# Performance work log

Hardware: AMD Instinct MI355X
Metric: run time of the kernel (lower is better)

## Reference

```python
import jax, jax.numpy as jnp
import numpy as np

N_NODES = 50000
N_EDGES = 1600000
EMB_DIM = 128
N_PATH = 2
N_LAYERS = 2
N_HEADS = 8
HEAD_DIM = EMB_DIM // N_HEADS


def setup_inputs() -> dict:
    key = jax.random.key(0)
    ks = jax.random.split(key, 6)
    fs = jax.random.normal(ks[0], (N_PATH, N_NODES, EMB_DIM), dtype=jnp.float32)
    W = jax.random.normal(ks[1], (N_PATH, N_LAYERS, EMB_DIM, EMB_DIM), dtype=jnp.float32) * (1.0 / np.sqrt(EMB_DIM))
    attn_l = jax.random.normal(ks[2], (N_PATH, N_LAYERS, N_HEADS, HEAD_DIM), dtype=jnp.float32) * 0.1
    attn_r = jax.random.normal(ks[3], (N_PATH, N_LAYERS, N_HEADS, HEAD_DIM), dtype=jnp.float32) * 0.1
    bias = jnp.zeros((N_PATH, N_LAYERS, EMB_DIM), dtype=jnp.float32)
    edges = jax.random.randint(ks[4], (N_PATH, 2, N_EDGES), 0, N_NODES, dtype=jnp.int32)
    return {"fs": fs, "W": W, "attn_l": attn_l, "attn_r": attn_r, "bias": bias, "edges": edges}


def gat_conv(h, src, dst, W, al, ar, b):
    # h: [N, F_in]; DGL GATConv, eval mode (dropout off), residual Identity, bias, ELU.
    N = h.shape[0]
    H, D = al.shape
    feat = (h @ W).reshape(N, H, D)                      # fc projection
    el = jnp.einsum('nhd,hd->nh', feat, al)              # [N, H]
    er = jnp.einsum('nhd,hd->nh', feat, ar)              # [N, H]
    e = jax.nn.leaky_relu(el[src] + er[dst], 0.2)        # [E, H]
    # edge softmax over incoming edges of each destination node
    emax = jax.ops.segment_max(e, dst, num_segments=N)   # [N, H], -inf for 0-in-degree
    emax = jnp.where(jnp.isfinite(emax), emax, 0.0)
    ex = jnp.exp(e - emax[dst])                          # [E, H]
    esum = jax.ops.segment_sum(ex, dst, num_segments=N)  # [N, H]
    alpha = ex / jnp.maximum(esum[dst], 1e-9)            # [E, H]
    msg = alpha[:, :, None] * feat[src]                  # [E, H, D]
    rst = jax.ops.segment_sum(msg, dst, num_segments=N)  # [N, H, D]
    rst = rst + h.reshape(N, H, D) + b.reshape(1, H, D)  # residual (Identity) + bias
    out = jax.nn.elu(rst)
    return out.reshape(N, H * D), alpha


def reference(fs, W, attn_l, attn_r, bias, edges):
    semantic_embeddings = []
    element_weights = []
    for p in range(N_PATH):
        h = fs[p]
        src, dst = edges[p, 0], edges[p, 1]
        attn = None
        for l in range(N_LAYERS):
            h, attn = gat_conv(h, src, dst, W[p, l], attn_l[p, l], attn_r[p, l], bias[p, l])
        semantic_embeddings.append(h)
        element_weights.append(attn)
    return jnp.stack(semantic_embeddings), jnp.stack(element_weights)
```

## Files before the change

kernel.cpp:

```cpp
#include <hip/hip_runtime.h>
#include <hip/hip_bf16.h>

#define NND 50000
#define NE  1600000
#define EMB 128
#define NH  8
#define HD  16
#define NB  98

typedef __attribute__((ext_vector_type(8))) short short8v;
typedef __attribute__((ext_vector_type(4))) float f32x4;

__device__ __forceinline__ float lrelu(float x) { return x > 0.f ? x : 0.2f * x; }
__device__ __forceinline__ float elu(float x)   { return x > 0.f ? x : expm1f(x); }

__device__ __forceinline__ unsigned short f2bf(float x) {
    __hip_bfloat16 b = __float2bfloat16(x);
    return *reinterpret_cast<unsigned short*>(&b);
}
__device__ __forceinline__ float bf2f(unsigned short u) {
    __hip_bfloat16 b = *reinterpret_cast<__hip_bfloat16*>(&u);
    return __bfloat162float(b);
}

__global__ __launch_bounds__(256) void wpack4(
    const float* __restrict__ W, unsigned short* __restrict__ bphi, unsigned short* __restrict__ bplo)
{
    int s = blockIdx.x * 256 + threadIdx.x;
    int q    = s >> 11;
    int sidx = s & 2047;
    int n    = sidx >> 8;
    int kt   = (sidx >> 6) & 3;
    int lane = sidx & 63;
    int col  = n * 16 + (lane & 15);
    int krow = kt * 32 + ((lane >> 4) << 3);
    const float* Wm = W + (size_t)q * EMB * EMB;
    #pragma unroll
    for (int j = 0; j < 8; ++j) {
        float x = Wm[(size_t)(krow + j) * EMB + col];
        unsigned short hi = f2bf(x);
        unsigned short lo = f2bf(x - bf2f(hi));
        bphi[(size_t)s * 8 + j] = hi;
        bplo[(size_t)s * 8 + j] = lo;
    }
}

__device__ __forceinline__ void gemm_epilogue(
    f32x4 acc[2][2], int lane, int wave, int rowbase,
    const float* __restrict__ alv, const float* __restrict__ arv,
    unsigned short* __restrict__ feat_bf, float* __restrict__ el, float* __restrict__ er)
{
    const int colr = lane & 15;
    const int rgrp = lane >> 4;
    #pragma unroll
    for (int m = 0; m < 2; ++m) {
        const int row0 = rowbase + m * 16 + rgrp * 4;
        #pragma unroll
        for (int q = 0; q < 2; ++q) {
            const int nn = wave * 2 + q;
            f32x4 a = acc[m][q];
            #pragma unroll
            for (int r = 0; r < 4; ++r) {
                if (row0 + r < NND)
                    feat_bf[(size_t)(row0 + r) * EMB + nn * 16 + colr] = f2bf(a[r]);
            }
            const float alc = alv[nn * 16 + colr];
            const float arc = arv[nn * 16 + colr];
            float pl[4], pr[4];
            #pragma unroll
            for (int r = 0; r < 4; ++r) { pl[r] = a[r] * alc; pr[r] = a[r] * arc; }
            #pragma unroll
            for (int mask = 1; mask < 16; mask <<= 1) {
                #pragma unroll
                for (int r = 0; r < 4; ++r) {
                    pl[r] += __shfl_xor(pl[r], mask);
                    pr[r] += __shfl_xor(pr[r], mask);
                }
            }
            if (colr == 0) {
                #pragma unroll
                for (int r = 0; r < 4; ++r) {
                    int row = row0 + r;
                    if (row < NND) {
                        el[row * NH + nn] = pl[r];
                        er[row * NH + nn] = pr[r];
                    }
                }
            }
        }
    }
}

__global__ __launch_bounds__(256) void mfma_gemm_f32(
    const float* __restrict__ fs,
    const unsigned short* __restrict__ bphi_all, const unsigned short* __restrict__ bplo_all,
    const float* __restrict__ al_all, const float* __restrict__ ar_all,
    unsigned short* __restrict__ feat_all, float* __restrict__ el_all, float* __restrict__ er_all)
{
    const int p = blockIdx.y;
    const int q4 = p * 2;
    const float* hin = fs + (size_t)p * NND * EMB;
    const unsigned short* bphi = bphi_all + (size_t)q4 * 16384;
    const unsigned short* bplo = bplo_all + (size_t)q4 * 16384;
    const float* alv = al_all + (size_t)q4 * NH * HD;
    const float* arv = ar_all + (size_t)q4 * NH * HD;
    unsigned short* feat_bf = feat_all + (size_t)p * NND * EMB;
    float* el = el_all + (size_t)p * NND * NH;
    float* er = er_all + (size_t)p * NND * NH;

    const int lane = threadIdx.x & 63;
    const int wave = threadIdx.x >> 6;
    const int rowbase = blockIdx.x * 32;

    f32x4 acc[2][2];
    #pragma unroll
    for (int m = 0; m < 2; ++m)
        #pragma unroll
        for (int q = 0; q < 2; ++q)
            acc[m][q] = (f32x4){0.f, 0.f, 0.f, 0.f};

    const int ar0 = rowbase + (lane & 15);
    const int ar1 = ar0 + 16;
    const int car0 = ar0 < NND ? ar0 : NND - 1;
    const int car1 = ar1 < NND ? ar1 : NND - 1;
    const int kofs = (lane >> 4) * 8;

    #pragma unroll
    for (int kt = 0; kt < 4; ++kt) {
        const int k0 = kt * 32 + kofs;
        short8v ah0, av0, ah1, av1;
        {
            const float4* fr = reinterpret_cast<const float4*>(hin + (size_t)car0 * EMB + k0);
            float4 x0 = fr[0], x1 = fr[1];
            float xs[8] = { x0.x, x0.y, x0.z, x0.w, x1.x, x1.y, x1.z, x1.w };
            #pragma unroll
            for (int j = 0; j < 8; ++j) {
                unsigned short hi = f2bf(xs[j]);
                ah0[j] = (short)hi;
                av0[j] = (short)f2bf(xs[j] - bf2f(hi));
            }
        }
        {
            const float4* fr = reinterpret_cast<const float4*>(hin + (size_t)car1 * EMB + k0);
            float4 x0 = fr[0], x1 = fr[1];
            float xs[8] = { x0.x, x0.y, x0.z, x0.w, x1.x, x1.y, x1.z, x1.w };
            #pragma unroll
            for (int j = 0; j < 8; ++j) {
                unsigned short hi = f2bf(xs[j]);
                ah1[j] = (short)hi;
                av1[j] = (short)f2bf(xs[j] - bf2f(hi));
            }
        }
        #pragma unroll
        for (int q = 0; q < 2; ++q) {
            const int nn = wave * 2 + q;
            const size_t bofs = ((size_t)(nn * 4 + kt) * 64 + lane) * 8;
            short8v bh = *reinterpret_cast<const short8v*>(bphi + bofs);
            short8v bl = *reinterpret_cast<const short8v*>(bplo + bofs);
            acc[0][q] = __builtin_amdgcn_mfma_f32_16x16x32_bf16(ah0, bh, acc[0][q], 0, 0, 0);
            acc[1][q] = __builtin_amdgcn_mfma_f32_16x16x32_bf16(ah1, bh, acc[1][q], 0, 0, 0);
            acc[0][q] = __builtin_amdgcn_mfma_f32_16x16x32_bf16(av0, bh, acc[0][q], 0, 0, 0);
            acc[1][q] = __builtin_amdgcn_mfma_f32_16x16x32_bf16(av1, bh, acc[1][q], 0, 0, 0);
            acc[0][q] = __builtin_amdgcn_mfma_f32_16x16x32_bf16(ah0, bl, acc[0][q], 0, 0, 0);
            acc[1][q] = __builtin_amdgcn_mfma_f32_16x16x32_bf16(ah1, bl, acc[1][q], 0, 0, 0);
        }
    }
    gemm_epilogue(acc, lane, wave, rowbase, alv, arv, feat_bf, el, er);
}

__global__ __launch_bounds__(256) void mfma_gemm_bf(
    const unsigned short* __restrict__ hhi_all, const unsigned short* __restrict__ hlo_all,
    const unsigned short* __restrict__ bphi_all, const unsigned short* __restrict__ bplo_all,
    const float* __restrict__ al_all, const float* __restrict__ ar_all,
    unsigned short* __restrict__ feat_all, float* __restrict__ el_all, float* __restrict__ er_all)
{
    const int p = blockIdx.y;
    const int q4 = p * 2 + 1;
    const unsigned short* hhi = hhi_all + (size_t)p * NND * EMB;
    const unsigned short* hlo = hlo_all + (size_t)p * NND * EMB;
    const unsigned short* bphi = bphi_all + (size_t)q4 * 16384;
    const unsigned short* bplo = bplo_all + (size_t)q4 * 16384;
    const float* alv = al_all + (size_t)q4 * NH * HD;
    const float* arv = ar_all + (size_t)q4 * NH * HD;
    unsigned short* feat_bf = feat_all + (size_t)p * NND * EMB;
    float* el = el_all + (size_t)p * NND * NH;
    float* er = er_all + (size_t)p * NND * NH;

    const int lane = threadIdx.x & 63;
    const int wave = threadIdx.x >> 6;
    const int rowbase = blockIdx.x * 32;

    f32x4 acc[2][2];
    #pragma unroll
    for (int m = 0; m < 2; ++m)
        #pragma unroll
        for (int q = 0; q < 2; ++q)
            acc[m][q] = (f32x4){0.f, 0.f, 0.f, 0.f};

    const int ar0 = rowbase + (lane & 15);
    const int ar1 = ar0 + 16;
    const int car0 = ar0 < NND ? ar0 : NND - 1;
    const int car1 = ar1 < NND ? ar1 : NND - 1;
    const int kofs = (lane >> 4) * 8;

    #pragma unroll
    for (int kt = 0; kt < 4; ++kt) {
        const int k0 = kt * 32 + kofs;
        short8v ah0 = *reinterpret_cast<const short8v*>(hhi + (size_t)car0 * EMB + k0);
        short8v av0 = *reinterpret_cast<const short8v*>(hlo + (size_t)car0 * EMB + k0);
        short8v ah1 = *reinterpret_cast<const short8v*>(hhi + (size_t)car1 * EMB + k0);
        short8v av1 = *reinterpret_cast<const short8v*>(hlo + (size_t)car1 * EMB + k0);
        #pragma unroll
        for (int q = 0; q < 2; ++q) {
            const int nn = wave * 2 + q;
            const size_t bofs = ((size_t)(nn * 4 + kt) * 64 + lane) * 8;
            short8v bh = *reinterpret_cast<const short8v*>(bphi + bofs);
            short8v bl = *reinterpret_cast<const short8v*>(bplo + bofs);
            acc[0][q] = __builtin_amdgcn_mfma_f32_16x16x32_bf16(ah0, bh, acc[0][q], 0, 0, 0);
            acc[1][q] = __builtin_amdgcn_mfma_f32_16x16x32_bf16(ah1, bh, acc[1][q], 0, 0, 0);
            acc[0][q] = __builtin_amdgcn_mfma_f32_16x16x32_bf16(av0, bh, acc[0][q], 0, 0, 0);
            acc[1][q] = __builtin_amdgcn_mfma_f32_16x16x32_bf16(av1, bh, acc[1][q], 0, 0, 0);
            acc[0][q] = __builtin_amdgcn_mfma_f32_16x16x32_bf16(ah0, bl, acc[0][q], 0, 0, 0);
            acc[1][q] = __builtin_amdgcn_mfma_f32_16x16x32_bf16(ah1, bl, acc[1][q], 0, 0, 0);
        }
    }
    gemm_epilogue(acc, lane, wave, rowbase, alv, arv, feat_bf, el, er);
}

__global__ __launch_bounds__(256) void bucket_count(
    const int* __restrict__ edges, int* __restrict__ bcnt)
{
    const int p = blockIdx.y;
    const int* dst = edges + (size_t)p * 2 * NE + NE;
    __shared__ int hist[NB];
    const int t = threadIdx.x;
    for (int b = t; b < NB; b += 256) hist[b] = 0;
    __syncthreads();
    const int e0 = blockIdx.x * 2048 + t * 8;
    #pragma unroll
    for (int j = 0; j < 8; ++j) {
        int e = e0 + j;
        if (e < NE) atomicAdd(&hist[dst[e] >> 9], 1);
    }
    __syncthreads();
    for (int b = t; b < NB; b += 256)
        if (hist[b]) atomicAdd(&bcnt[p * 128 + b], hist[b]);
}

__global__ __launch_bounds__(128) void scan_bucket(
    const int* __restrict__ bcnt, int* __restrict__ bbase, int* __restrict__ bcur)
{
    const int p = blockIdx.x;
    __shared__ int s[128];
    const int t = threadIdx.x;
    s[t] = (t < NB) ? bcnt[p * 128 + t] : 0;
    __syncthreads();
    for (int off = 1; off < 128; off <<= 1) {
        int v = (t >= off) ? s[t - off] : 0;
        __syncthreads();
        s[t] += v;
        __syncthreads();
    }
    int excl = (t > 0) ? s[t - 1] : 0;
    if (t <= NB) bbase[p * 128 + t] = excl;
    if (t < NB)  bcur[p * 128 + t]  = excl;
}

__global__ __launch_bounds__(256) void bucket_scatter(
    const int* __restrict__ edges, int* __restrict__ bcur, int* __restrict__ ebuf)
{
    const int p = blockIdx.y;
    const int* src = edges + (size_t)p * 2 * NE;
    const int* dst = src + NE;
    int* eb = ebuf + (size_t)p * NE;
    __shared__ int hist[NB];
    __shared__ int base[NB];
    __shared__ int lcur[NB];
    const int t  = threadIdx.x;
    const int e0 = blockIdx.x * 2048 + t * 8;

    for (int b = t; b < NB; b += 256) { hist[b] = 0; lcur[b] = 0; }
    __syncthreads();

    int sj[8], dj[8];
    bool vj[8];
    #pragma unroll
    for (int j = 0; j < 8; ++j) {
        int e = e0 + j;
        vj[j] = (e < NE);
        if (vj[j]) {
            sj[j] = src[e];
            dj[j] = dst[e];
            atomicAdd(&hist[dj[j] >> 9], 1);
        }
    }
    __syncthreads();
    for (int b = t; b < NB; b += 256) {
        int c = hist[b];
        base[b] = c > 0 ? atomicAdd(&bcur[p * 128 + b], c) : 0;
    }
    __syncthreads();
    #pragma unroll
    for (int j = 0; j < 8; ++j) {
        if (vj[j]) {
            int b   = dj[j] >> 9;
            int off = atomicAdd(&lcur[b], 1);
            eb[(size_t)base[b] + off] = (sj[j] << 9) | (dj[j] & 511);
        }
    }
}

__global__ __launch_bounds__(1024) void bucket_fill(
    const int* __restrict__ bbase, const int* __restrict__ ebuf,
    int* __restrict__ rowptr, int* __restrict__ csrsrc)
{
    const int p = blockIdx.y;
    const int* eb = ebuf + (size_t)p * NE;
    int* rp = rowptr + (size_t)p * (NND + 1);
    int* cs = csrsrc + (size_t)p * NE;
    __shared__ int hist[512];
    __shared__ int excl[512];
    const int b    = blockIdx.x;
    const int n0   = b << 9;
    const int t    = threadIdx.x;
    const int base = bbase[p * 128 + b];
    const int cnt  = bbase[p * 128 + b + 1] - base;

    if (t < 512) hist[t] = 0;
    __syncthreads();
    for (int i = t; i < cnt; i += 1024)
        atomicAdd(&hist[eb[base + i] & 511], 1);
    __syncthreads();
    if (t < 512) excl[t] = hist[t];
    __syncthreads();
    for (int off = 1; off < 512; off <<= 1) {
        int v = 0;
        if (t < 512 && t >= off) v = excl[t - off];
        __syncthreads();
        if (t < 512) excl[t] += v;
        __syncthreads();
    }
    if (t < 512) {
        int e = excl[t] - hist[t];
        int n = n0 + t;
        if (n < NND) rp[n] = base + e;
        hist[t] = e;
    }
    if (b == NB - 1 && t == 0) rp[NND] = NE;
    __syncthreads();
    for (int i = t; i < cnt; i += 1024) {
        int ed = eb[base + i];
        int q = atomicAdd(&hist[ed & 511], 1);
        cs[base + q] = ed >> 9;
    }
}

__global__ __launch_bounds__(256) void gather_agg(
    const int* __restrict__ rowptr_all, const int* __restrict__ csrsrc_all,
    const float* __restrict__ el_all, const float* __restrict__ er_all,
    const unsigned int* __restrict__ feat_all,
    const float* __restrict__ fs,
    const unsigned int* __restrict__ hhi_all,
    const unsigned int* __restrict__ hlo_all,
    const float* __restrict__ bias_all,
    float* __restrict__ esum_all,
    float* __restrict__ out_emb,
    int layer)
{
    const int p    = blockIdx.y;
    const int wid  = (blockIdx.x * blockDim.x + threadIdx.x) >> 6;
    const int lane = threadIdx.x & 63;
    if (wid >= NND) return;
    const int n = wid;
    const int h = lane >> 3;

    const int* rowptr = rowptr_all + (size_t)p * (NND + 1);
    const int* csrsrc = csrsrc_all + (size_t)p * NE;
    const float* el   = el_all + (size_t)p * NND * NH;
    const float* er   = er_all + (size_t)p * NND * NH;
    const unsigned int* featu = feat_all + (size_t)p * NND * 64;
    const float* bias = bias_all + (size_t)(p * 2 + layer) * EMB;

    const float ern = er[n * NH + h];
    const int r0 = __builtin_amdgcn_readfirstlane(rowptr[n]);
    const int r1 = __builtin_amdgcn_readfirstlane(rowptr[n + 1]);

    float acc0 = 0.f, acc1 = 0.f, es = 0.f;

    int i = r0;
    for (; i + 16 <= r1; i += 16) {
        int sj[16];
        #pragma unroll
        for (int j = 0; j < 16; ++j) sj[j] = csrsrc[i + j];
        unsigned int vs[16];
        #pragma unroll
        for (int j = 0; j < 16; ++j) vs[j] = featu[(size_t)sj[j] * 64 + lane];
        float w[16];
        #pragma unroll
        for (int j = 0; j < 16; ++j) w[j] = __expf(lrelu(el[sj[j] * NH + h] + ern));
        #pragma unroll
        for (int j = 0; j < 16; ++j) {
            es  += w[j];
            acc0 = fmaf(w[j], __uint_as_float(vs[j] << 16), acc0);
            acc1 = fmaf(w[j], __uint_as_float(vs[j] & 0xffff0000u), acc1);
        }
    }
    if (i + 8 <= r1) {
        int sj[8];
        #pragma unroll
        for (int j = 0; j < 8; ++j) sj[j] = csrsrc[i + j];
        unsigned int vs[8];
        #pragma unroll
        for (int j = 0; j < 8; ++j) vs[j] = featu[(size_t)sj[j] * 64 + lane];
        #pragma unroll
        for (int j = 0; j < 8; ++j) {
            float w = __expf(lrelu(el[sj[j] * NH + h] + ern));
            es  += w;
            acc0 = fmaf(w, __uint_as_float(vs[j] << 16), acc0);
            acc1 = fmaf(w, __uint_as_float(vs[j] & 0xffff0000u), acc1);
        }
        i += 8;
    }
    for (; i < r1; ++i) {
        int sj = csrsrc[i];
        unsigned int v = featu[(size_t)sj * 64 + lane];
        float w = __expf(lrelu(el[sj * NH + h] + ern));
        es  += w;
        acc0 = fmaf(w, __uint_as_float(v << 16), acc0);
        acc1 = fmaf(w, __uint_as_float(v & 0xffff0000u), acc1);
    }

    if ((lane & 7) == 0) esum_all[((size_t)p * NND + n) * NH + h] = es;
    const float inv = 1.f / fmaxf(es, 1e-9f);

    float h0, h1;
    if (layer == 0) {
        float2 hv = reinterpret_cast<const float2*>(fs + (size_t)p * NND * EMB)[(size_t)n * 64 + lane];
        h0 = hv.x; h1 = hv.y;
    } else {
        unsigned int hiu = hhi_all[((size_t)p * NND + n) * 64 + lane];
        unsigned int lou = hlo_all[((size_t)p * NND + n) * 64 + lane];
        h0 = __uint_as_float(hiu << 16) + __uint_as_float(lou << 16);
        h1 = __uint_as_float(hiu & 0xffff0000u) + __uint_as_float(lou & 0xffff0000u);
    }
    float o0 = elu(fmaf(acc0, inv, h0 + bias[lane * 2]));
    float o1 = elu(fmaf(acc1, inv, h1 + bias[lane * 2 + 1]));

    if (layer == 1) {
        reinterpret_cast<float2*>(out_emb + (size_t)p * NND * EMB)[(size_t)n * 64 + lane] =
            make_float2(o0, o1);
    } else {
        unsigned short hi0 = f2bf(o0), hi1 = f2bf(o1);
        unsigned short lo0 = f2bf(o0 - bf2f(hi0)), lo1 = f2bf(o1 - bf2f(hi1));
        const size_t idx = ((size_t)p * NND + n) * 64 + lane;
        const_cast<unsigned int*>(hhi_all)[idx] = (unsigned int)hi0 | ((unsigned int)hi1 << 16);
        const_cast<unsigned int*>(hlo_all)[idx] = (unsigned int)lo0 | ((unsigned int)lo1 << 16);
    }
}

__global__ __launch_bounds__(256) void alpha_write8(
    const int* __restrict__ edges,
    const float* __restrict__ el_all, const float* __restrict__ er_all,
    const float* __restrict__ esum_all, float* __restrict__ out_alpha)
{
    const int p = blockIdx.y;
    int e = blockIdx.x * 256 + threadIdx.x;
    if (e >= NE) return;
    const int* src = edges + (size_t)p * 2 * NE;
    const int* dst = src + NE;
    const float* el   = el_all   + (size_t)p * NND * NH;
    const float* er   = er_all   + (size_t)p * NND * NH;
    const float* esum = esum_all + (size_t)p * NND * NH;
    int s = src[e], d = dst[e];
    const float4* el4 = reinterpret_cast<const float4*>(el + (size_t)s * 8);
    const float4* er4 = reinterpret_cast<const float4*>(er + (size_t)d * 8);
    const float4* es4 = reinterpret_cast<const float4*>(esum + (size_t)d * 8);
    float4 L0 = el4[0], L1 = el4[1];
    float4 R0 = er4[0], R1 = er4[1];
    float4 S0 = es4[0], S1 = es4[1];
    float4 a0, a1;
    a0.x = __fdividef(__expf(lrelu(L0.x + R0.x)), fmaxf(S0.x, 1e-9f));
    a0.y = __fdividef(__expf(lrelu(L0.y + R0.y)), fmaxf(S0.y, 1e-9f));
    a0.z = __fdividef(__expf(lrelu(L0.z + R0.z)), fmaxf(S0.z, 1e-9f));
    a0.w = __fdividef(__expf(lrelu(L0.w + R0.w)), fmaxf(S0.w, 1e-9f));
    a1.x = __fdividef(__expf(lrelu(L1.x + R1.x)), fmaxf(S1.x, 1e-9f));
    a1.y = __fdividef(__expf(lrelu(L1.y + R1.y)), fmaxf(S1.y, 1e-9f));
    a1.z = __fdividef(__expf(lrelu(L1.z + R1.z)), fmaxf(S1.z, 1e-9f));
    a1.w = __fdividef(__expf(lrelu(L1.w + R1.w)), fmaxf(S1.w, 1e-9f));
    float4* o4 = reinterpret_cast<float4*>(out_alpha + ((size_t)p * NE + e) * 8);
    o4[0] = a0;
    o4[1] = a1;
}

extern "C" void kernel_launch(void* const* d_in, const int* in_sizes, int n_in,
                              void* d_out, int out_size, void* d_ws, size_t ws_size,
                              hipStream_t stream) {
    const float* fs   = (const float*)d_in[0];
    const float* W    = (const float*)d_in[1];
    const float* al   = (const float*)d_in[2];
    const float* ar   = (const float*)d_in[3];
    const float* bias = (const float*)d_in[4];
    const int*   edges= (const int*)d_in[5];

    float* out       = (float*)d_out;
    float* out_emb   = out;
    float* out_alpha = out + (size_t)2 * NND * EMB;

    char* ws = (char*)d_ws;
    auto take = [&](size_t bytes) {
        char* r = ws;
        ws += (bytes + 15) & ~(size_t)15;
        return r;
    };
    unsigned short* feat_bf = (unsigned short*)take((size_t)2 * NND * EMB * 2);
    unsigned short* hhi     = (unsigned short*)take((size_t)2 * NND * EMB * 2);
    unsigned short* hlo     = (unsigned short*)take((size_t)2 * NND * EMB * 2);
    float*          el      = (float*)take((size_t)2 * NND * NH * 4);
    float*          er      = (float*)take((size_t)2 * NND * NH * 4);
    float*          esum    = (float*)take((size_t)2 * NND * NH * 4);
    int*            rowptr  = (int*)take((size_t)2 * (NND + 1) * 4);
    int*            bcnt    = (int*)take((size_t)2 * 128 * 4);
    int*            bbase   = (int*)take((size_t)2 * 128 * 4);
    int*            bcur    = (int*)take((size_t)2 * 128 * 4);
    int*            csrsrc  = (int*)take((size_t)2 * NE * 4);
    unsigned short* bphi    = (unsigned short*)take((size_t)4 * 16384 * 2);
    unsigned short* bplo    = (unsigned short*)take((size_t)4 * 16384 * 2);

    int*          ebuf  = (int*)hlo;
    unsigned int* featu = (unsigned int*)feat_bf;
    unsigned int* hhi_u = (unsigned int*)hhi;
    unsigned int* hlo_u = (unsigned int*)hlo;

    hipMemsetAsync(bcnt, 0, (size_t)2 * 128 * 4, stream);
    bucket_count<<<dim3((NE + 2047) / 2048, 2), 256, 0, stream>>>(edges, bcnt);
    scan_bucket<<<2, 128, 0, stream>>>(bcnt, bbase, bcur);
    bucket_scatter<<<dim3((NE + 2047) / 2048, 2), 256, 0, stream>>>(edges, bcur, ebuf);
    bucket_fill<<<dim3(NB, 2), 1024, 0, stream>>>(bbase, ebuf, rowptr, csrsrc);

    wpack4<<<32, 256, 0, stream>>>(W, bphi, bplo);

    mfma_gemm_f32<<<dim3((NND + 31) / 32, 2), 256, 0, stream>>>(
        fs, bphi, bplo, al, ar, feat_bf, el, er);
    gather_agg<<<dim3((NND + 3) / 4, 2), 256, 0, stream>>>(
        rowptr, csrsrc, el, er, featu, fs, hhi_u, hlo_u, bias, esum, nullptr, 0);

    mfma_gemm_bf<<<dim3((NND + 31) / 32, 2), 256, 0, stream>>>(
        hhi, hlo, bphi, bplo, al, ar, feat_bf, el, er);
    gather_agg<<<dim3((NND + 3) / 4, 2), 256, 0, stream>>>(
        rowptr, csrsrc, el, er, featu, fs, hhi_u, hlo_u, bias, esum, out_emb, 1);
    alpha_write8<<<dim3((NE + 255) / 256, 2), 256, 0, stream>>>(
        edges, el, er, esum, out_alpha);
}
```

Measured before the change: 578.6 us.

## Split edge-weight exponentials into a separate pass and store features as fp16

Adds a wexp_pass kernel per layer that computes the unnormalised edge attention weights in CSR order, stores them as fp16 in a new workspace buffer and writes esum. gather_agg then reads these precomputed weights instead of gathering el and recomputing exp for each of the 8 lanes sharing a head. Projected features switch from bf16 to fp16 storage for better precision. The cost is an extra kernel launch per layer plus writing and reading about 51 MB of fp16 weights.

```diff
diff --git a/kernel.cpp b/kernel.cpp
--- a/kernel.cpp
+++ b/kernel.cpp
@@ -1,5 +1,6 @@
 #include <hip/hip_runtime.h>
 #include <hip/hip_bf16.h>
+#include <hip/hip_fp16.h>
 
 #define NND 50000
 #define NE  1600000
@@ -48,7 +49,7 @@
 __device__ __forceinline__ void gemm_epilogue(
     f32x4 acc[2][2], int lane, int wave, int rowbase,
     const float* __restrict__ alv, const float* __restrict__ arv,
-    unsigned short* __restrict__ feat_bf, float* __restrict__ el, float* __restrict__ er)
+    unsigned short* __restrict__ feat_f16, float* __restrict__ el, float* __restrict__ er)
 {
     const int colr = lane & 15;
     const int rgrp = lane >> 4;
@@ -62,7 +63,8 @@
             #pragma unroll
             for (int r = 0; r < 4; ++r) {
                 if (row0 + r < NND)
-                    feat_bf[(size_t)(row0 + r) * EMB + nn * 16 + colr] = f2bf(a[r]);
+                    feat_f16[(size_t)(row0 + r) * EMB + nn * 16 + colr] =
+                        __half_as_ushort(__float2half(a[r]));
             }
             const float alc = alv[nn * 16 + colr];
             const float arc = arv[nn * 16 + colr];
@@ -104,7 +106,7 @@
     const unsigned short* bplo = bplo_all + (size_t)q4 * 16384;
     const float* alv = al_all + (size_t)q4 * NH * HD;
     const float* arv = ar_all + (size_t)q4 * NH * HD;
-    unsigned short* feat_bf = feat_all + (size_t)p * NND * EMB;
+    unsigned short* feat_f16 = feat_all + (size_t)p * NND * EMB;
     float* el = el_all + (size_t)p * NND * NH;
     float* er = er_all + (size_t)p * NND * NH;
 
@@ -165,7 +167,7 @@
             acc[1][q] = __builtin_amdgcn_mfma_f32_16x16x32_bf16(ah1, bl, acc[1][q], 0, 0, 0);
         }
     }
-    gemm_epilogue(acc, lane, wave, rowbase, alv, arv, feat_bf, el, er);
+    gemm_epilogue(acc, lane, wave, rowbase, alv, arv, feat_f16, el, er);
 }
 
 __global__ __launch_bounds__(256) void mfma_gemm_bf(
@@ -182,7 +184,7 @@
     const unsigned short* bplo = bplo_all + (size_t)q4 * 16384;
     const float* alv = al_all + (size_t)q4 * NH * HD;
     const float* arv = ar_all + (size_t)q4 * NH * HD;
-    unsigned short* feat_bf = feat_all + (size_t)p * NND * EMB;
+    unsigned short* feat_f16 = feat_all + (size_t)p * NND * EMB;
     float* el = el_all + (size_t)p * NND * NH;
     float* er = er_all + (size_t)p * NND * NH;
 
@@ -224,7 +226,7 @@
             acc[1][q] = __builtin_amdgcn_mfma_f32_16x16x32_bf16(ah1, bl, acc[1][q], 0, 0, 0);
         }
     }
-    gemm_epilogue(acc, lane, wave, rowbase, alv, arv, feat_bf, el, er);
+    gemm_epilogue(acc, lane, wave, rowbase, alv, arv, feat_f16, el, er);
 }
 
 __global__ __launch_bounds__(256) void bucket_count(
@@ -355,15 +357,54 @@
     }
 }
 
+__global__ __launch_bounds__(256) void wexp_pass(
+    const int* __restrict__ rowptr_all, const int* __restrict__ csrsrc_all,
+    const float* __restrict__ el_all, const float* __restrict__ er_all,
+    unsigned short* __restrict__ wexp_all, float* __restrict__ esum_all)
+{
+    const int p    = blockIdx.y;
+    const int wid  = (blockIdx.x * blockDim.x + threadIdx.x) >> 6;
+    const int lane = threadIdx.x & 63;
+    if (wid >= NND) return;
+    const int n  = wid;
+    const int h  = lane >> 3;
+    const int j8 = lane & 7;
+
+    const int* rowptr = rowptr_all + (size_t)p * (NND + 1);
+    const int* csrsrc = csrsrc_all + (size_t)p * NE;
+    const float* el   = el_all + (size_t)p * NND * NH;
+    const float* er   = er_all + (size_t)p * NND * NH;
+    unsigned short* wexp = wexp_all + (size_t)p * NE * NH;
+
+    const float ern = er[n * NH + h];
+    const int r0 = __builtin_amdgcn_readfirstlane(rowptr[n]);
+    const int r1 = __builtin_amdgcn_readfirstlane(rowptr[n + 1]);
+
+    float esp = 0.f;
+    for (int i = r0; i < r1; i += 16) {
+        int i0 = i + j8, i1 = i + j8 + 8;
+        bool v0 = i0 < r1, v1 = i1 < r1;
+        int s0 = csrsrc[v0 ? i0 : r0];
+        int s1 = csrsrc[v1 ? i1 : r0];
+        float w0 = __expf(lrelu(el[s0 * NH + h] + ern));
+        float w1 = __expf(lrelu(el[s1 * NH + h] + ern));
+        if (v0) { esp += w0; wexp[(size_t)i0 * NH + h] = __half_as_ushort(__float2half(w0)); }
+        if (v1) { esp += w1; wexp[(size_t)i1 * NH + h] = __half_as_ushort(__float2half(w1)); }
+    }
+    esp += __shfl_xor(esp, 1);
+    esp += __shfl_xor(esp, 2);
+    esp += __shfl_xor(esp, 4);
+    if (j8 == 0) esum_all[((size_t)p * NND + n) * NH + h] = esp;
+}
+
 __global__ __launch_bounds__(256) void gather_agg(
     const int* __restrict__ rowptr_all, const int* __restrict__ csrsrc_all,
-    const float* __restrict__ el_all, const float* __restrict__ er_all,
+    const unsigned short* __restrict__ wexp_all, const float* __restrict__ esum_all,
     const unsigned int* __restrict__ feat_all,
     const float* __restrict__ fs,
     const unsigned int* __restrict__ hhi_all,
     const unsigned int* __restrict__ hlo_all,
     const float* __restrict__ bias_all,
-    float* __restrict__ esum_all,
     float* __restrict__ out_emb,
     int layer)
 {
@@ -376,16 +417,14 @@
 
     const int* rowptr = rowptr_all + (size_t)p * (NND + 1);
     const int* csrsrc = csrsrc_all + (size_t)p * NE;
-    const float* el   = el_all + (size_t)p * NND * NH;
-    const float* er   = er_all + (size_t)p * NND * NH;
+    const unsigned short* wexp = wexp_all + (size_t)p * NE * NH;
     const unsigned int* featu = feat_all + (size_t)p * NND * 64;
     const float* bias = bias_all + (size_t)(p * 2 + layer) * EMB;
 
-    const float ern = er[n * NH + h];
     const int r0 = __builtin_amdgcn_readfirstlane(rowptr[n]);
     const int r1 = __builtin_amdgcn_readfirstlane(rowptr[n + 1]);
 
-    float acc0 = 0.f, acc1 = 0.f, es = 0.f;
+    float acc0 = 0.f, acc1 = 0.f;
 
     int i = r0;
     for (; i + 16 <= r1; i += 16) {
@@ -395,14 +434,15 @@
         unsigned int vs[16];
         #pragma unroll
         for (int j = 0; j < 16; ++j) vs[j] = featu[(size_t)sj[j] * 64 + lane];
-        float w[16];
-        #pragma unroll
-        for (int j = 0; j < 16; ++j) w[j] = __expf(lrelu(el[sj[j] * NH + h] + ern));
+        unsigned short wu[16];
+        #pragma unroll
+        for (int j = 0; j < 16; ++j) wu[j] = wexp[(size_t)(i + j) * NH + h];
         #pragma unroll
         for (int j = 0; j < 16; ++j) {
-            es  += w[j];
-            acc0 = fmaf(w[j], __uint_as_float(vs[j] << 16), acc0);
-            acc1 = fmaf(w[j], __uint_as_float(vs[j] & 0xffff0000u), acc1);
+            float w = __half2float(__ushort_as_half(wu[j]));
+            __half2 v = *reinterpret_cast<__half2*>(&vs[j]);
+            acc0 = fmaf(w, __half2float(__low2half(v)), acc0);
+            acc1 = fmaf(w, __half2float(__high2half(v)), acc1);
         }
     }
     if (i + 8 <= r1) {
@@ -412,25 +452,28 @@
         unsigned int vs[8];
         #pragma unroll
         for (int j = 0; j < 8; ++j) vs[j] = featu[(size_t)sj[j] * 64 + lane];
+        unsigned short wu[8];
+        #pragma unroll
+        for (int j = 0; j < 8; ++j) wu[j] = wexp[(size_t)(i + j) * NH + h];
         #pragma unroll
         for (int j = 0; j < 8; ++j) {
-            float w = __expf(lrelu(el[sj[j] * NH + h] + ern));
-            es  += w;
-            acc0 = fmaf(w, __uint_as_float(vs[j] << 16), acc0);
-            acc1 = fmaf(w, __uint_as_float(vs[j] & 0xffff0000u), acc1);
+            float w = __half2float(__ushort_as_half(wu[j]));
+            __half2 v = *reinterpret_cast<__half2*>(&vs[j]);
+            acc0 = fmaf(w, __half2float(__low2half(v)), acc0);
+            acc1 = fmaf(w, __half2float(__high2half(v)), acc1);
         }
         i += 8;
     }
     for (; i < r1; ++i) {
         int sj = csrsrc[i];
-        unsigned int v = featu[(size_t)sj * 64 + lane];
-        float w = __expf(lrelu(el[sj * NH + h] + ern));
-        es  += w;
-        acc0 = fmaf(w, __uint_as_float(v << 16), acc0);
-        acc1 = fmaf(w, __uint_as_float(v & 0xffff0000u), acc1);
-    }
-
-    if ((lane & 7) == 0) esum_all[((size_t)p * NND + n) * NH + h] = es;
+        unsigned int vraw = featu[(size_t)sj * 64 + lane];
+        float w = __half2float(__ushort_as_half(wexp[(size_t)i * NH + h]));
+        __half2 v = *reinterpret_cast<__half2*>(&vraw);
+        acc0 = fmaf(w, __half2float(__low2half(v)), acc0);
+        acc1 = fmaf(w, __half2float(__high2half(v)), acc1);
+    }
+
+    const float es  = esum_all[((size_t)p * NND + n) * NH + h];
     const float inv = 1.f / fmaxf(es, 1e-9f);
 
     float h0, h1;
@@ -512,22 +555,23 @@
         ws += (bytes + 15) & ~(size_t)15;
         return r;
     };
-    unsigned short* feat_bf = (unsigned short*)take((size_t)2 * NND * EMB * 2);
-    unsigned short* hhi     = (unsigned short*)take((size_t)2 * NND * EMB * 2);
-    unsigned short* hlo     = (unsigned short*)take((size_t)2 * NND * EMB * 2);
-    float*          el      = (float*)take((size_t)2 * NND * NH * 4);
-    float*          er      = (float*)take((size_t)2 * NND * NH * 4);
-    float*          esum    = (float*)take((size_t)2 * NND * NH * 4);
-    int*            rowptr  = (int*)take((size_t)2 * (NND + 1) * 4);
-    int*            bcnt    = (int*)take((size_t)2 * 128 * 4);
-    int*            bbase   = (int*)take((size_t)2 * 128 * 4);
-    int*            bcur    = (int*)take((size_t)2 * 128 * 4);
-    int*            csrsrc  = (int*)take((size_t)2 * NE * 4);
-    unsigned short* bphi    = (unsigned short*)take((size_t)4 * 16384 * 2);
-    unsigned short* bplo    = (unsigned short*)take((size_t)4 * 16384 * 2);
+    unsigned short* feat_f16 = (unsigned short*)take((size_t)2 * NND * EMB * 2);
+    unsigned short* hhi      = (unsigned short*)take((size_t)2 * NND * EMB * 2);
+    unsigned short* hlo      = (unsigned short*)take((size_t)2 * NND * EMB * 2);
+    float*          el       = (float*)take((size_t)2 * NND * NH * 4);
+    float*          er       = (float*)take((size_t)2 * NND * NH * 4);
+    float*          esum     = (float*)take((size_t)2 * NND * NH * 4);
+    int*            rowptr   = (int*)take((size_t)2 * (NND + 1) * 4);
+    int*            bcnt     = (int*)take((size_t)2 * 128 * 4);
+    int*            bbase    = (int*)take((size_t)2 * 128 * 4);
+    int*            bcur     = (int*)take((size_t)2 * 128 * 4);
+    int*            csrsrc   = (int*)take((size_t)2 * NE * 4);
+    unsigned short* wexp     = (unsigned short*)take((size_t)2 * NE * NH * 2);
+    unsigned short* bphi     = (unsigned short*)take((size_t)4 * 16384 * 2);
+    unsigned short* bplo     = (unsigned short*)take((size_t)4 * 16384 * 2);
 
     int*          ebuf  = (int*)hlo;
-    unsigned int* featu = (unsigned int*)feat_bf;
+    unsigned int* featu = (unsigned int*)feat_f16;
     unsigned int* hhi_u = (unsigned int*)hhi;
     unsigned int* hlo_u = (unsigned int*)hlo;
 
@@ -540,14 +584,18 @@
     wpack4<<<32, 256, 0, stream>>>(W, bphi, bplo);
 
     mfma_gemm_f32<<<dim3((NND + 31) / 32, 2), 256, 0, stream>>>(
-        fs, bphi, bplo, al, ar, feat_bf, el, er);
+        fs, bphi, bplo, al, ar, feat_f16, el, er);
+    wexp_pass<<<dim3((NND + 3) / 4, 2), 256, 0, stream>>>(
+        rowptr, csrsrc, el, er, wexp, esum);
     gather_agg<<<dim3((NND + 3) / 4, 2), 256, 0, stream>>>(
-        rowptr, csrsrc, el, er, featu, fs, hhi_u, hlo_u, bias, esum, nullptr, 0);
+        rowptr, csrsrc, wexp, esum, featu, fs, hhi_u, hlo_u, bias, nullptr, 0);
 
     mfma_gemm_bf<<<dim3((NND + 31) / 32, 2), 256, 0, stream>>>(
-        hhi, hlo, bphi, bplo, al, ar, feat_bf, el, er);
+        hhi, hlo, bphi, bplo, al, ar, feat_f16, el, er);
+    wexp_pass<<<dim3((NND + 3) / 4, 2), 256, 0, stream>>>(
+        rowptr, csrsrc, el, er, wexp, esum);
     gather_agg<<<dim3((NND + 3) / 4, 2), 256, 0, stream>>>(
-        rowptr, csrsrc, el, er, featu, fs, hhi_u, hlo_u, bias, esum, out_emb, 1);
+        rowptr, csrsrc, wexp, esum, featu, fs, hhi_u, hlo_u, bias, out_emb, 1);
     alpha_write8<<<dim3((NE + 255) / 256, 2), 256, 0, stream>>>(
         edges, el, er, esum, out_alpha);
 }
```

New measurement: 663.5 us. 14.7% more time.
